# Optimization experiments

Hardware: AMD Instinct MI355X
Metric: run time of the kernel (lower is better)

## Reference

```python
import jax, jax.numpy as jnp
import numpy as np

N = 100000
E = 1600000
D_IN = 128
D_OUT = 128


def setup_inputs() -> dict:
    key = jax.random.key(0)
    k1, k2, k3, k4, k5, k6 = jax.random.split(key, 6)
    h = jax.random.normal(k1, (N, D_IN), dtype=jnp.float32)
    # deg^{-1/2}-style positive per-node normalization, shape [N,1]
    norm = jax.random.uniform(k2, (N, 1), dtype=jnp.float32, minval=0.05, maxval=1.0)
    weight = jax.random.normal(k3, (D_IN, D_OUT), dtype=jnp.float32) * (1.0 / np.sqrt(D_IN))
    bias = jax.random.normal(k4, (D_OUT,), dtype=jnp.float32) * 0.01
    src = jax.random.randint(k5, (E,), 0, N, dtype=jnp.int32)
    dst = jax.random.randint(k6, (E,), 0, N, dtype=jnp.int32)
    return {"h": h, "norm": norm, "weight": weight, "bias": bias, "src": src, "dst": dst}


def reference(h, norm, weight, bias, src, dst):
    # m = (h @ W) * norm   (per-source-node message)
    m = jnp.matmul(h, weight) * norm            # [N, D_OUT]
    # copy_src + sum: scatter-sum messages from src nodes into dst nodes
    n = jax.ops.segment_sum(m[src], dst, num_segments=h.shape[0])  # [N, D_OUT]
    # destination-side normalization, bias, LeakyReLU(0.2)
    n = n * norm + bias
    return jax.nn.leaky_relu(n, negative_slope=0.2)
```

## Files before the change

kernel.cpp:

```cpp
#include <hip/hip_runtime.h>

#define N_NODES 100000
#define E_EDGES 1600000
#define D 128
#define SHIFT 7
#define BNODES 128
#define NB ((N_NODES + BNODES - 1) / BNODES)

#define CNT_CHUNK 2048
#define CNT_NBLK ((E_EDGES + CNT_CHUNK - 1) / CNT_CHUNK)
#define PREP_NBLK (N_NODES * 32 / 256)
#define SCAT_CHUNK 16384
#define SCAT_NBLK ((E_EDGES + SCAT_CHUNK - 1) / SCAT_CHUNK)
#define GATH_NBLK (N_NODES / 16)
#define GATH32_NBLK (N_NODES / 8)

#define GROWS 64
#define KCH 32

typedef _Float16       f16x8  __attribute__((ext_vector_type(8)));
typedef float          f32x4  __attribute__((ext_vector_type(4)));
typedef unsigned short u16x8  __attribute__((ext_vector_type(8)));

#define WS_CNT   0
#define WS_BOFF  784
#define WS_POS   1568
#define WS_NOFF  2352
#define WS_EBUF  102400
#define WS_ESRC  (102400 + E_EDGES)
#define WS_HS    (102400 + 2 * E_EDGES)
#define WS_FULL_INTS ((size_t)WS_HS + (size_t)N_NODES * D / 2)
#define WS_MID_INTS  ((size_t)WS_HS)

__global__ __launch_bounds__(256) void prep_count(const float* __restrict__ h,
                                                  const float* __restrict__ norm,
                                                  unsigned short* __restrict__ hs,
                                                  const int* __restrict__ dst,
                                                  int* __restrict__ cnt,
                                                  int prep_blocks) {
    __shared__ int hist[NB];
    const int t = threadIdx.x;
    if ((int)blockIdx.x < prep_blocks) {
        const int idx = blockIdx.x * 256 + t;
        const int node = idx >> 5;
        const int c = (idx & 31) << 2;
        const float nv = norm[node];
        const float4 v = *reinterpret_cast<const float4*>(h + node * D + c);
        float a[4] = {v.x * nv, v.y * nv, v.z * nv, v.w * nv};
        ushort4 o;
        unsigned short* op = reinterpret_cast<unsigned short*>(&o);
        #pragma unroll
        for (int i = 0; i < 4; ++i) {
            unsigned int u = __float_as_uint(a[i]);
            u += 0x7FFFu + ((u >> 16) & 1u);
            op[i] = (unsigned short)(u >> 16);
        }
        *reinterpret_cast<ushort4*>(hs + node * D + c) = o;
        return;
    }
    const int cb = blockIdx.x - prep_blocks;
    const int e0 = cb * CNT_CHUNK;
    const int rem = (E_EDGES - e0 < CNT_CHUNK) ? (E_EDGES - e0) : CNT_CHUNK;
    for (int i = t; i < NB; i += 256) hist[i] = 0;
    __syncthreads();
    if (rem == CNT_CHUNK) {
        const int4* d4 = reinterpret_cast<const int4*>(dst + e0);
        #pragma unroll
        for (int p = 0; p < 2; ++p) {
            const int4 v = d4[p * 256 + t];
            atomicAdd(&hist[v.x >> SHIFT], 1);
            atomicAdd(&hist[v.y >> SHIFT], 1);
            atomicAdd(&hist[v.z >> SHIFT], 1);
            atomicAdd(&hist[v.w >> SHIFT], 1);
        }
    } else {
        for (int i = t; i < rem; i += 256)
            atomicAdd(&hist[dst[e0 + i] >> SHIFT], 1);
    }
    __syncthreads();
    for (int b = t; b < NB; b += 256) {
        const int c = hist[b];
        if (c) atomicAdd(&cnt[b], c);
    }
}

__global__ __launch_bounds__(1024) void coarse_scan(const int* __restrict__ cnt,
                                                    int* __restrict__ boff,
                                                    int* __restrict__ pos) {
    __shared__ int buf[2][1024];
    const int t = threadIdx.x;
    const int v = (t < NB) ? cnt[t] : 0;
    int pi = 0;
    buf[0][t] = v;
    __syncthreads();
    #pragma unroll
    for (int o = 1; o < 1024; o <<= 1) {
        const int nv = buf[pi][t] + (t >= o ? buf[pi][t - o] : 0);
        buf[1 - pi][t] = nv;
        pi = 1 - pi;
        __syncthreads();
    }
    if (t < NB) {
        const int excl = buf[pi][t] - v;
        boff[t] = excl;
        pos[t] = excl;
    }
    if (t == 0) boff[NB] = E_EDGES;
}

__global__ __launch_bounds__(1024) void coarse_scatter(const int* __restrict__ src,
                                                       const int* __restrict__ dst,
                                                       int* __restrict__ pos,
                                                       int* __restrict__ ebuf) {
    __shared__ int hist[NB];
    const int t = threadIdx.x;
    const int e0 = blockIdx.x * SCAT_CHUNK;
    const int rem = (E_EDGES - e0 < SCAT_CHUNK) ? (E_EDGES - e0) : SCAT_CHUNK;
    for (int i = t; i < NB; i += 1024) hist[i] = 0;
    __syncthreads();
    if (rem == SCAT_CHUNK) {
        const int4* d4 = reinterpret_cast<const int4*>(dst + e0);
        #pragma unroll
        for (int p = 0; p < 4; ++p) {
            const int4 v = d4[p * 1024 + t];
            atomicAdd(&hist[v.x >> SHIFT], 1);
            atomicAdd(&hist[v.y >> SHIFT], 1);
            atomicAdd(&hist[v.z >> SHIFT], 1);
            atomicAdd(&hist[v.w >> SHIFT], 1);
        }
    } else {
        for (int i = t; i < rem; i += 1024)
            atomicAdd(&hist[dst[e0 + i] >> SHIFT], 1);
    }
    __syncthreads();
    for (int b = t; b < NB; b += 1024) {
        const int c = hist[b];
        if (c) hist[b] = atomicAdd(&pos[b], c);
    }
    __syncthreads();
    if (rem == SCAT_CHUNK) {
        const int4* d4 = reinterpret_cast<const int4*>(dst + e0);
        const int4* s4 = reinterpret_cast<const int4*>(src + e0);
        #pragma unroll
        for (int p = 0; p < 4; ++p) {
            const int4 dv = d4[p * 1024 + t];
            const int4 sv = s4[p * 1024 + t];
            int pz;
            pz = atomicAdd(&hist[dv.x >> SHIFT], 1);
            ebuf[pz] = (sv.x << SHIFT) | (dv.x & (BNODES - 1));
            pz = atomicAdd(&hist[dv.y >> SHIFT], 1);
            ebuf[pz] = (sv.y << SHIFT) | (dv.y & (BNODES - 1));
            pz = atomicAdd(&hist[dv.z >> SHIFT], 1);
            ebuf[pz] = (sv.z << SHIFT) | (dv.z & (BNODES - 1));
            pz = atomicAdd(&hist[dv.w >> SHIFT], 1);
            ebuf[pz] = (sv.w << SHIFT) | (dv.w & (BNODES - 1));
        }
    } else {
        for (int i = t; i < rem; i += 1024) {
            const int d = dst[e0 + i];
            const int b = d >> SHIFT;
            const int p = atomicAdd(&hist[b], 1);
            ebuf[p] = (src[e0 + i] << SHIFT) | (d & (BNODES - 1));
        }
    }
}

__global__ __launch_bounds__(256) void bin_sort(const int* __restrict__ boff,
                                                const int* __restrict__ ebuf,
                                                int* __restrict__ esrc,
                                                int* __restrict__ noff) {
    __shared__ int hist[BNODES];
    __shared__ int curs[BNODES];
    __shared__ int sbuf[2][BNODES];
    const int t = threadIdx.x;
    const int bin = blockIdx.x;
    if (t < BNODES) hist[t] = 0;
    __syncthreads();
    const int b0 = boff[bin];
    const int b1 = boff[bin + 1];
    for (int i = b0 + t; i < b1; i += 256)
        atomicAdd(&hist[ebuf[i] & (BNODES - 1)], 1);
    __syncthreads();
    if (t < BNODES) sbuf[0][t] = hist[t];
    __syncthreads();
    int pi = 0;
    #pragma unroll
    for (int o = 1; o < BNODES; o <<= 1) {
        if (t < BNODES)
            sbuf[1 - pi][t] = sbuf[pi][t] + (t >= o ? sbuf[pi][t - o] : 0);
        pi = 1 - pi;
        __syncthreads();
    }
    if (t < BNODES) {
        const int base = b0 + sbuf[pi][t] - hist[t];
        curs[t] = base;
        const int node = (bin << SHIFT) + t;
        if (node < N_NODES) noff[node] = base;
    }
    if (bin == 0 && t == 0) noff[N_NODES] = E_EDGES;
    __syncthreads();
    for (int i = b0 + t; i < b1; i += 256) {
        const int w = ebuf[i];
        const int p = atomicAdd(&curs[w & (BNODES - 1)], 1);
        esrc[p] = w >> SHIFT;
    }
}

__device__ __forceinline__ void wprep_body(int tid, const float* __restrict__ Wm,
                                           f16x8* __restrict__ Whs) {
    const int kiter = tid >> 9;
    const int nt = (tid >> 6) & 7;
    const int lane = tid & 63;
    const int q = lane >> 4;
    const int col = nt * 16 + (lane & 15);
    f16x8 v;
    #pragma unroll
    for (int j = 0; j < 8; ++j)
        v[j] = (_Float16)Wm[(kiter * 32 + q * 8 + j) * D + col];
    Whs[tid] = v;
}

__global__ __launch_bounds__(256) void gather_wprep(
    const unsigned short* __restrict__ hs, const int* __restrict__ noff,
    const int* __restrict__ esrc, float* __restrict__ g,
    const float* __restrict__ Wm, f16x8* __restrict__ Whs)
{
    if ((int)blockIdx.x >= GATH_NBLK) {
        wprep_body((blockIdx.x - GATH_NBLK) * 256 + threadIdx.x, Wm, Whs);
        return;
    }
    const int t = threadIdx.x;
    const int node = blockIdx.x * 16 + (t >> 4);
    const int c = (t & 15) << 3;
    const int beg = noff[node];
    const int end = noff[node + 1];
    float a[8];
    #pragma unroll
    for (int j = 0; j < 8; ++j) a[j] = 0.f;
    int i = beg;
    for (; i + 3 < end; i += 4) {
        const int s0 = esrc[i];
        const int s1 = esrc[i + 1];
        const int s2 = esrc[i + 2];
        const int s3 = esrc[i + 3];
        const u16x8 u0 = *reinterpret_cast<const u16x8*>(hs + s0 * D + c);
        const u16x8 u1 = *reinterpret_cast<const u16x8*>(hs + s1 * D + c);
        const u16x8 u2 = *reinterpret_cast<const u16x8*>(hs + s2 * D + c);
        const u16x8 u3 = *reinterpret_cast<const u16x8*>(hs + s3 * D + c);
        #pragma unroll
        for (int j = 0; j < 8; ++j) {
            a[j] += __uint_as_float((unsigned int)u0[j] << 16);
            a[j] += __uint_as_float((unsigned int)u1[j] << 16);
            a[j] += __uint_as_float((unsigned int)u2[j] << 16);
            a[j] += __uint_as_float((unsigned int)u3[j] << 16);
        }
    }
    for (; i < end; ++i) {
        const int s = esrc[i];
        const u16x8 u = *reinterpret_cast<const u16x8*>(hs + s * D + c);
        #pragma unroll
        for (int j = 0; j < 8; ++j)
            a[j] += __uint_as_float((unsigned int)u[j] << 16);
    }
    float4 v0, v1;
    v0.x = a[0]; v0.y = a[1]; v0.z = a[2]; v0.w = a[3];
    v1.x = a[4]; v1.y = a[5]; v1.z = a[6]; v1.w = a[7];
    *reinterpret_cast<float4*>(g + node * D + c) = v0;
    *reinterpret_cast<float4*>(g + node * D + c + 4) = v1;
}

__global__ __launch_bounds__(256) void gather_fp32(const float* __restrict__ h,
                                                   const float* __restrict__ norm,
                                                   const int* __restrict__ noff,
                                                   const int* __restrict__ esrc,
                                                   float* __restrict__ g,
                                                   const float* __restrict__ Wm,
                                                   f16x8* __restrict__ Whs) {
    if ((int)blockIdx.x >= GATH32_NBLK) {
        wprep_body((blockIdx.x - GATH32_NBLK) * 256 + threadIdx.x, Wm, Whs);
        return;
    }
    const int t = threadIdx.x;
    const int node = blockIdx.x * 8 + (t >> 5);
    const int c = (t & 31) << 2;
    const int beg = noff[node];
    const int end = noff[node + 1];
    float4 acc = make_float4(0.f, 0.f, 0.f, 0.f);
    for (int i = beg; i < end; ++i) {
        const int s = esrc[i];
        const float nv = norm[s];
        const float4 hv = *reinterpret_cast<const float4*>(h + s * D + c);
        acc.x += hv.x * nv;
        acc.y += hv.y * nv;
        acc.z += hv.z * nv;
        acc.w += hv.w * nv;
    }
    *reinterpret_cast<float4*>(g + node * D + c) = acc;
}

__global__ __launch_bounds__(256) void scatter_kernel(
    const float* __restrict__ h, const float* __restrict__ norm,
    const int* __restrict__ src, const int* __restrict__ dst,
    float* __restrict__ g)
{
    const int idx = blockIdx.x * 256 + threadIdx.x;
    const int e = idx >> 5;
    const int c = (idx & 31) << 2;
    const int s = src[e];
    const int d = dst[e];
    const float nv = norm[s];
    const float4 hv = *reinterpret_cast<const float4*>(h + s * D + c);
    float* gp = g + d * D + c;
    atomicAdd(gp + 0, hv.x * nv);
    atomicAdd(gp + 1, hv.y * nv);
    atomicAdd(gp + 2, hv.z * nv);
    atomicAdd(gp + 3, hv.w * nv);
}

__global__ __launch_bounds__(256) void gemm_mfma(
    float* __restrict__ out, const f16x8* __restrict__ Whs,
    const float* __restrict__ bias, const float* __restrict__ norm)
{
    __shared__ f16x8 Wlds[2048];
    const int t = threadIdx.x;
    const int row0 = blockIdx.x * 64;

    #pragma unroll
    for (int p = 0; p < 8; ++p)
        reinterpret_cast<float4*>(Wlds)[p * 256 + t] =
            reinterpret_cast<const float4*>(Whs)[p * 256 + t];
    __syncthreads();

    const int lane = t & 63;
    const int strip = t >> 6;
    const int q = lane >> 4;
    const int l15 = lane & 15;

    int mrow = row0 + strip * 16 + l15;
    if (mrow >= N_NODES) mrow = N_NODES - 1;

    f32x4 acc[8];
    #pragma unroll
    for (int i = 0; i < 8; ++i) acc[i] = (f32x4){0.f, 0.f, 0.f, 0.f};

    #pragma unroll
    for (int kiter = 0; kiter < 4; ++kiter) {
        const float* gp = out + mrow * D + kiter * 32 + q * 8;
        const float4 ga = *reinterpret_cast<const float4*>(gp);
        const float4 gb = *reinterpret_cast<const float4*>(gp + 4);
        f16x8 a;
        a[0] = (_Float16)ga.x; a[1] = (_Float16)ga.y;
        a[2] = (_Float16)ga.z; a[3] = (_Float16)ga.w;
        a[4] = (_Float16)gb.x; a[5] = (_Float16)gb.y;
        a[6] = (_Float16)gb.z; a[7] = (_Float16)gb.w;
        #pragma unroll
        for (int nt = 0; nt < 8; ++nt) {
            const f16x8 b = Wlds[(kiter * 8 + nt) * 64 + lane];
            acc[nt] = __builtin_amdgcn_mfma_f32_16x16x32_f16(a, b, acc[nt], 0, 0, 0);
        }
    }

    float nrm[4];
    int mr[4];
    #pragma unroll
    for (int rgi = 0; rgi < 4; ++rgi) {
        mr[rgi] = row0 + strip * 16 + q * 4 + rgi;
        nrm[rgi] = (mr[rgi] < N_NODES) ? norm[mr[rgi]] : 0.f;
    }
    #pragma unroll
    for (int nt = 0; nt < 8; ++nt) {
        const int col = nt * 16 + l15;
        const float bc = bias[col];
        #pragma unroll
        for (int rgi = 0; rgi < 4; ++rgi) {
            if (mr[rgi] < N_NODES) {
                float v = acc[nt][rgi] * nrm[rgi] + bc;
                v = v > 0.f ? v : 0.2f * v;
                out[mr[rgi] * D + col] = v;
            }
        }
    }
}

__global__ __launch_bounds__(256) void gemm_epilogue(
    float* __restrict__ out, const float* __restrict__ Wm,
    const float* __restrict__ bias, const float* __restrict__ norm)
{
    __shared__ float gs[GROWS][D + 4];
    __shared__ float Wlds[KCH][D];
    const int t = threadIdx.x;
    const int row0 = blockIdx.x * GROWS;

    #pragma unroll
    for (int p = 0; p < 8; ++p) {
        const int i = p * 256 + t;
        const int r = i >> 5;
        const int c = (i & 31) << 2;
        int gr = row0 + r;
        if (gr >= N_NODES) gr = N_NODES - 1;
        const float4 v = *reinterpret_cast<const float4*>(out + gr * D + c);
        *reinterpret_cast<float4*>(&gs[r][c]) = v;
    }

    const int rg = (t >> 5) * 8;
    const int cb = (t & 31) << 2;

    float4 acc[8];
    #pragma unroll
    for (int i = 0; i < 8; ++i) acc[i] = make_float4(0.f, 0.f, 0.f, 0.f);

    for (int kc = 0; kc < D; kc += KCH) {
        __syncthreads();
        #pragma unroll
        for (int p = 0; p < 4; ++p) {
            const int i = p * 256 + t;
            const int kk = i >> 5;
            const int c = (i & 31) << 2;
            *reinterpret_cast<float4*>(&Wlds[kk][c]) =
                *reinterpret_cast<const float4*>(Wm + (kc + kk) * D + c);
        }
        __syncthreads();

        #pragma unroll
        for (int k4 = 0; k4 < KCH; k4 += 4) {
            float4 wv[4];
            #pragma unroll
            for (int kk = 0; kk < 4; ++kk)
                wv[kk] = *reinterpret_cast<const float4*>(&Wlds[k4 + kk][cb]);
            #pragma unroll
            for (int i = 0; i < 8; ++i) {
                const float4 gv = *reinterpret_cast<const float4*>(&gs[rg + i][kc + k4]);
                acc[i].x += gv.x * wv[0].x; acc[i].y += gv.x * wv[0].y;
                acc[i].z += gv.x * wv[0].z; acc[i].w += gv.x * wv[0].w;
                acc[i].x += gv.y * wv[1].x; acc[i].y += gv.y * wv[1].y;
                acc[i].z += gv.y * wv[1].z; acc[i].w += gv.y * wv[1].w;
                acc[i].x += gv.z * wv[2].x; acc[i].y += gv.z * wv[2].y;
                acc[i].z += gv.z * wv[2].z; acc[i].w += gv.z * wv[2].w;
                acc[i].x += gv.w * wv[3].x; acc[i].y += gv.w * wv[3].y;
                acc[i].z += gv.w * wv[3].z; acc[i].w += gv.w * wv[3].w;
            }
        }
    }

    const float4 b = *reinterpret_cast<const float4*>(bias + cb);
    #pragma unroll
    for (int i = 0; i < 8; ++i) {
        const int gr = row0 + rg + i;
        if (gr < N_NODES) {
            const float nv = norm[gr];
            float4 v;
            v.x = acc[i].x * nv + b.x;
            v.y = acc[i].y * nv + b.y;
            v.z = acc[i].z * nv + b.z;
            v.w = acc[i].w * nv + b.w;
            v.x = v.x > 0.f ? v.x : 0.2f * v.x;
            v.y = v.y > 0.f ? v.y : 0.2f * v.y;
            v.z = v.z > 0.f ? v.z : 0.2f * v.z;
            v.w = v.w > 0.f ? v.w : 0.2f * v.w;
            *reinterpret_cast<float4*>(out + gr * D + cb) = v;
        }
    }
}

extern "C" void kernel_launch(void* const* d_in, const int* in_sizes, int n_in,
                              void* d_out, int out_size, void* d_ws, size_t ws_size,
                              hipStream_t stream) {
    const float* h    = (const float*)d_in[0];
    const float* norm = (const float*)d_in[1];
    const float* Wm   = (const float*)d_in[2];
    const float* bias = (const float*)d_in[3];
    const int*   src  = (const int*)d_in[4];
    const int*   dst  = (const int*)d_in[5];
    float* out = (float*)d_out;
    int* ws = (int*)d_ws;

    if (ws_size >= WS_MID_INTS * 4) {
        int* cnt  = ws + WS_CNT;
        int* boff = ws + WS_BOFF;
        int* pos  = ws + WS_POS;
        int* noff = ws + WS_NOFF;
        int* ebuf = ws + WS_EBUF;
        int* esrc = ws + WS_ESRC;
        unsigned short* hs = (unsigned short*)(ws + WS_HS);
        f16x8* Whs = (f16x8*)ebuf;
        const bool use_bf16 = (ws_size >= WS_FULL_INTS * 4);

        hipMemsetAsync(cnt, 0, NB * sizeof(int), stream);
        if (use_bf16) {
            prep_count<<<PREP_NBLK + CNT_NBLK, 256, 0, stream>>>(h, norm, hs, dst, cnt, PREP_NBLK);
        } else {
            prep_count<<<CNT_NBLK, 256, 0, stream>>>(h, norm, hs, dst, cnt, 0);
        }
        coarse_scan   <<<1, 1024, 0, stream>>>(cnt, boff, pos);
        coarse_scatter<<<SCAT_NBLK, 1024, 0, stream>>>(src, dst, pos, ebuf);
        bin_sort      <<<NB, 256, 0, stream>>>(boff, ebuf, esrc, noff);
        if (use_bf16)
            gather_wprep<<<GATH_NBLK + 8, 256, 0, stream>>>(hs, noff, esrc, out, Wm, Whs);
        else
            gather_fp32<<<GATH32_NBLK + 8, 256, 0, stream>>>(h, norm, noff, esrc, out, Wm, Whs);
        gemm_mfma<<<(N_NODES + 63) / 64, 256, 0, stream>>>(out, Whs, bias, norm);
    } else {
        hipMemsetAsync(out, 0, (size_t)N_NODES * D * sizeof(float), stream);
        scatter_kernel<<<(E_EDGES * 32) / 256, 256, 0, stream>>>(h, norm, src, dst, out);
        gemm_epilogue<<<(N_NODES + GROWS - 1) / GROWS, 256, 0, stream>>>(out, Wm, bias, norm);
    }
}
```

Baseline: 255.5 us.

## Fuse neighbor gather with MFMA GEMM epilogue and halve scatter chunk size

Replaces the separate gather kernel and GEMM kernel with one kernel. Each block gathers 64 destination rows into fp16 LDS, converts W into LDS, and runs MFMA with the norm/bias/LeakyReLU epilogue. This removes the fp32 intermediate round-trip through global memory and one launch. The gather loop is also unrolled to 8 edges, and the coarse scatter chunk is halved to launch more blocks. The cost is that every block rebuilds W in LDS, the intermediate is rounded to fp16 before the matmul, and LDS use limits occupancy during the latency-bound gather.

```diff
diff --git a/kernel.cpp b/kernel.cpp
--- a/kernel.cpp
+++ b/kernel.cpp
@@ -10,10 +10,13 @@
 #define CNT_CHUNK 2048
 #define CNT_NBLK ((E_EDGES + CNT_CHUNK - 1) / CNT_CHUNK)
 #define PREP_NBLK (N_NODES * 32 / 256)
-#define SCAT_CHUNK 16384
+#define SCAT_CHUNK 8192
+#define SCAT_PASS 2
 #define SCAT_NBLK ((E_EDGES + SCAT_CHUNK - 1) / SCAT_CHUNK)
-#define GATH_NBLK (N_NODES / 16)
 #define GATH32_NBLK (N_NODES / 8)
+
+#define FBLK 64
+#define FGRID ((N_NODES + FBLK - 1) / FBLK)
 
 #define GROWS 64
 #define KCH 32
@@ -121,7 +124,7 @@
     if (rem == SCAT_CHUNK) {
         const int4* d4 = reinterpret_cast<const int4*>(dst + e0);
         #pragma unroll
-        for (int p = 0; p < 4; ++p) {
+        for (int p = 0; p < SCAT_PASS; ++p) {
             const int4 v = d4[p * 1024 + t];
             atomicAdd(&hist[v.x >> SHIFT], 1);
             atomicAdd(&hist[v.y >> SHIFT], 1);
@@ -142,7 +145,7 @@
         const int4* d4 = reinterpret_cast<const int4*>(dst + e0);
         const int4* s4 = reinterpret_cast<const int4*>(src + e0);
         #pragma unroll
-        for (int p = 0; p < 4; ++p) {
+        for (int p = 0; p < SCAT_PASS; ++p) {
             const int4 dv = d4[p * 1024 + t];
             const int4 sv = s4[p * 1024 + t];
             int pz;
@@ -220,53 +223,138 @@
     Whs[tid] = v;
 }
 
-__global__ __launch_bounds__(256) void gather_wprep(
+__global__ __launch_bounds__(256) void fused_gather_gemm(
     const unsigned short* __restrict__ hs, const int* __restrict__ noff,
-    const int* __restrict__ esrc, float* __restrict__ g,
-    const float* __restrict__ Wm, f16x8* __restrict__ Whs)
+    const int* __restrict__ esrc, const float* __restrict__ Wm,
+    const float* __restrict__ bias, const float* __restrict__ norm,
+    float* __restrict__ out)
 {
-    if ((int)blockIdx.x >= GATH_NBLK) {
-        wprep_body((blockIdx.x - GATH_NBLK) * 256 + threadIdx.x, Wm, Whs);
-        return;
-    }
-    const int t = threadIdx.x;
-    const int node = blockIdx.x * 16 + (t >> 4);
+    __shared__ _Float16 gs[FBLK][136];
+    __shared__ f16x8 Wlds[2048];
+    const int t = threadIdx.x;
+    const int row0 = blockIdx.x * FBLK;
     const int c = (t & 15) << 3;
-    const int beg = noff[node];
-    const int end = noff[node + 1];
-    float a[8];
-    #pragma unroll
-    for (int j = 0; j < 8; ++j) a[j] = 0.f;
-    int i = beg;
-    for (; i + 3 < end; i += 4) {
-        const int s0 = esrc[i];
-        const int s1 = esrc[i + 1];
-        const int s2 = esrc[i + 2];
-        const int s3 = esrc[i + 3];
-        const u16x8 u0 = *reinterpret_cast<const u16x8*>(hs + s0 * D + c);
-        const u16x8 u1 = *reinterpret_cast<const u16x8*>(hs + s1 * D + c);
-        const u16x8 u2 = *reinterpret_cast<const u16x8*>(hs + s2 * D + c);
-        const u16x8 u3 = *reinterpret_cast<const u16x8*>(hs + s3 * D + c);
-        #pragma unroll
-        for (int j = 0; j < 8; ++j) {
-            a[j] += __uint_as_float((unsigned int)u0[j] << 16);
-            a[j] += __uint_as_float((unsigned int)u1[j] << 16);
-            a[j] += __uint_as_float((unsigned int)u2[j] << 16);
-            a[j] += __uint_as_float((unsigned int)u3[j] << 16);
-        }
-    }
-    for (; i < end; ++i) {
-        const int s = esrc[i];
-        const u16x8 u = *reinterpret_cast<const u16x8*>(hs + s * D + c);
+
+    #pragma unroll 1
+    for (int r = 0; r < 4; ++r) {
+        const int nl = r * 16 + (t >> 4);
+        const int node = row0 + nl;
+        float a[8];
+        #pragma unroll
+        for (int j = 0; j < 8; ++j) a[j] = 0.f;
+        if (node < N_NODES) {
+            int i = noff[node];
+            const int end = noff[node + 1];
+            for (; i + 7 < end; i += 8) {
+                const int s0 = esrc[i];     const int s1 = esrc[i + 1];
+                const int s2 = esrc[i + 2]; const int s3 = esrc[i + 3];
+                const int s4 = esrc[i + 4]; const int s5 = esrc[i + 5];
+                const int s6 = esrc[i + 6]; const int s7 = esrc[i + 7];
+                const u16x8 u0 = *reinterpret_cast<const u16x8*>(hs + s0 * D + c);
+                const u16x8 u1 = *reinterpret_cast<const u16x8*>(hs + s1 * D + c);
+                const u16x8 u2 = *reinterpret_cast<const u16x8*>(hs + s2 * D + c);
+                const u16x8 u3 = *reinterpret_cast<const u16x8*>(hs + s3 * D + c);
+                const u16x8 u4 = *reinterpret_cast<const u16x8*>(hs + s4 * D + c);
+                const u16x8 u5 = *reinterpret_cast<const u16x8*>(hs + s5 * D + c);
+                const u16x8 u6 = *reinterpret_cast<const u16x8*>(hs + s6 * D + c);
+                const u16x8 u7 = *reinterpret_cast<const u16x8*>(hs + s7 * D + c);
+                #pragma unroll
+                for (int j = 0; j < 8; ++j) {
+                    a[j] += __uint_as_float((unsigned int)u0[j] << 16);
+                    a[j] += __uint_as_float((unsigned int)u1[j] << 16);
+                    a[j] += __uint_as_float((unsigned int)u2[j] << 16);
+                    a[j] += __uint_as_float((unsigned int)u3[j] << 16);
+                    a[j] += __uint_as_float((unsigned int)u4[j] << 16);
+                    a[j] += __uint_as_float((unsigned int)u5[j] << 16);
+                    a[j] += __uint_as_float((unsigned int)u6[j] << 16);
+                    a[j] += __uint_as_float((unsigned int)u7[j] << 16);
+                }
+            }
+            if (i + 3 < end) {
+                const int s0 = esrc[i];     const int s1 = esrc[i + 1];
+                const int s2 = esrc[i + 2]; const int s3 = esrc[i + 3];
+                const u16x8 u0 = *reinterpret_cast<const u16x8*>(hs + s0 * D + c);
+                const u16x8 u1 = *reinterpret_cast<const u16x8*>(hs + s1 * D + c);
+                const u16x8 u2 = *reinterpret_cast<const u16x8*>(hs + s2 * D + c);
+                const u16x8 u3 = *reinterpret_cast<const u16x8*>(hs + s3 * D + c);
+                #pragma unroll
+                for (int j = 0; j < 8; ++j) {
+                    a[j] += __uint_as_float((unsigned int)u0[j] << 16);
+                    a[j] += __uint_as_float((unsigned int)u1[j] << 16);
+                    a[j] += __uint_as_float((unsigned int)u2[j] << 16);
+                    a[j] += __uint_as_float((unsigned int)u3[j] << 16);
+                }
+                i += 4;
+            }
+            for (; i < end; ++i) {
+                const int s = esrc[i];
+                const u16x8 u = *reinterpret_cast<const u16x8*>(hs + s * D + c);
+                #pragma unroll
+                for (int j = 0; j < 8; ++j)
+                    a[j] += __uint_as_float((unsigned int)u[j] << 16);
+            }
+        }
+        f16x8 o;
+        #pragma unroll
+        for (int j = 0; j < 8; ++j) o[j] = (_Float16)a[j];
+        *reinterpret_cast<f16x8*>(&gs[nl][c]) = o;
+    }
+
+    #pragma unroll 1
+    for (int e = t; e < 2048; e += 256) {
+        const int kiter = e >> 9;
+        const int nt = (e >> 6) & 7;
+        const int lane = e & 63;
+        const int q = lane >> 4;
+        const int col = nt * 16 + (lane & 15);
+        f16x8 v;
         #pragma unroll
         for (int j = 0; j < 8; ++j)
-            a[j] += __uint_as_float((unsigned int)u[j] << 16);
-    }
-    float4 v0, v1;
-    v0.x = a[0]; v0.y = a[1]; v0.z = a[2]; v0.w = a[3];
-    v1.x = a[4]; v1.y = a[5]; v1.z = a[6]; v1.w = a[7];
-    *reinterpret_cast<float4*>(g + node * D + c) = v0;
-    *reinterpret_cast<float4*>(g + node * D + c + 4) = v1;
+            v[j] = (_Float16)Wm[(kiter * 32 + q * 8 + j) * D + col];
+        Wlds[e] = v;
+    }
+    __syncthreads();
+
+    const int lane = t & 63;
+    const int strip = t >> 6;
+    const int q = lane >> 4;
+    const int l15 = lane & 15;
+
+    f32x4 acc[8];
+    #pragma unroll
+    for (int i = 0; i < 8; ++i) acc[i] = (f32x4){0.f, 0.f, 0.f, 0.f};
+
+    #pragma unroll
+    for (int kiter = 0; kiter < 4; ++kiter) {
+        const f16x8 a =
+            *reinterpret_cast<const f16x8*>(&gs[strip * 16 + l15][kiter * 32 + q * 8]);
+        #pragma unroll
+        for (int nt = 0; nt < 8; ++nt) {
+            const f16x8 b = Wlds[(kiter * 8 + nt) * 64 + lane];
+            acc[nt] = __builtin_amdgcn_mfma_f32_16x16x32_f16(a, b, acc[nt], 0, 0, 0);
+        }
+    }
+
+    float nrm[4];
+    int mr[4];
+    #pragma unroll
+    for (int rgi = 0; rgi < 4; ++rgi) {
+        mr[rgi] = row0 + strip * 16 + q * 4 + rgi;
+        nrm[rgi] = (mr[rgi] < N_NODES) ? norm[mr[rgi]] : 0.f;
+    }
+    #pragma unroll
+    for (int nt = 0; nt < 8; ++nt) {
+        const int col = nt * 16 + l15;
+        const float bc = bias[col];
+        #pragma unroll
+        for (int rgi = 0; rgi < 4; ++rgi) {
+            if (mr[rgi] < N_NODES) {
+                float v = acc[nt][rgi] * nrm[rgi] + bc;
+                v = v > 0.f ? v : 0.2f * v;
+                out[mr[rgi] * D + col] = v;
+            }
+        }
+    }
 }
 
 __global__ __launch_bounds__(256) void gather_fp32(const float* __restrict__ h,
@@ -494,11 +582,12 @@
         coarse_scan   <<<1, 1024, 0, stream>>>(cnt, boff, pos);
         coarse_scatter<<<SCAT_NBLK, 1024, 0, stream>>>(src, dst, pos, ebuf);
         bin_sort      <<<NB, 256, 0, stream>>>(boff, ebuf, esrc, noff);
-        if (use_bf16)
-            gather_wprep<<<GATH_NBLK + 8, 256, 0, stream>>>(hs, noff, esrc, out, Wm, Whs);
-        else
+        if (use_bf16) {
+            fused_gather_gemm<<<FGRID, 256, 0, stream>>>(hs, noff, esrc, Wm, bias, norm, out);
+        } else {
             gather_fp32<<<GATH32_NBLK + 8, 256, 0, stream>>>(h, norm, noff, esrc, out, Wm, Whs);
-        gemm_mfma<<<(N_NODES + 63) / 64, 256, 0, stream>>>(out, Whs, bias, norm);
+            gemm_mfma<<<(N_NODES + 63) / 64, 256, 0, stream>>>(out, Whs, bias, norm);
+        }
     } else {
         hipMemsetAsync(out, 0, (size_t)N_NODES * D * sizeof(float), stream);
         scatter_kernel<<<(E_EDGES * 32) / 256, 256, 0, stream>>>(h, norm, src, dst, out);
```

New measurement: 255.6 us. No clear change (+0.1%).
